# Kernel tuning notes

Hardware: AMD Instinct MI355X
Metric: run time of the kernel (lower is better)

The kernel has to match this reference:

```python
import jax, jax.numpy as jnp
import numpy as np

B, S, I, F = 2048, 512, 256, 256  # batch, seq_length, input_size, filter_num


def setup_inputs() -> dict:
    key = jax.random.key(0)
    ks = jax.random.split(key, 9)
    sc = 0.05
    return {
        "hidden": jax.random.normal(ks[0], (B, I), jnp.float32),
        "inp": jax.random.normal(ks[1], (B, S, I), jnp.float32),
        "W1": jax.random.normal(ks[2], (F, I), jnp.float32) * sc,   # linear1 weight (no bias)
        "Wc": jax.random.normal(ks[3], (F, S), jnp.float32) * sc,   # conv kernel [F,1,S,1] squeezed
        "bc": jax.random.normal(ks[4], (F,), jnp.float32) * sc,     # conv bias
        "W2": jax.random.normal(ks[5], (I, I + F), jnp.float32) * sc,
        "b2": jax.random.normal(ks[6], (I,), jnp.float32) * sc,
        "Wfc": jax.random.normal(ks[7], (1, I), jnp.float32) * sc,
        "bfc": jax.random.normal(ks[8], (1,), jnp.float32) * sc,
    }


def reference(hidden, inp, W1, Wc, bc, W2, b2, Wfc, bfc):
    # w = linear1(hidden).unsqueeze(1): [B,1,F]
    w = hidden @ W1.T  # [B,F]
    # Conv2d(1,F,kernel=(S,1)) over input [B,1,S,I] -> [B,F,1,I]; kernel spans full
    # time axis with width 1, so it's a contraction over t per input channel i.
    Hc_raw = jnp.einsum('bti,ft->bfi', inp, Wc) + bc[None, :, None]  # [B,F,I]
    # faithful to torch: .squeeze().reshape([-1, input_size, filter_num])
    H_c = Hc_raw.reshape(-1, I, F)  # [B,I,F]
    s = jnp.sum(H_c * w[:, None, :], axis=2)          # [B,I]
    a = jax.nn.sigmoid(s)
    v = jnp.sum(a[:, :, None] * H_c, axis=1)          # [B,F]
    concat = jnp.concatenate([hidden, v], axis=1)     # [B,I+F]
    h_prime = concat @ W2.T + b2                      # [B,I]
    out = h_prime @ Wfc.T + bfc                       # [B,1]
    return out
```

## Files before the change

kernel.cpp:

```cpp
#include <hip/hip_runtime.h>

#define B_ 2048
#define S_ 512
#define I_ 256
#define F_ 256
#define NG 8

#define OFF_W    0
#define OFF_SW   (OFF_W + B_*F_)
#define OFF_U    (OFF_SW + B_)
#define OFF_P    (OFF_U + B_*S_)
#define OFF_RP   (OFF_P + B_*S_)

__global__ __launch_bounds__(256) void k_pre(
    const float* __restrict__ hidden, const float* __restrict__ W1,
    const float* __restrict__ W2, const float* __restrict__ Wfc,
    float* __restrict__ ws) {
  const int tid = threadIdx.x;

  if (blockIdx.x >= B_ / 4) {
    const int g = blockIdx.x - B_ / 4;
    float acc0 = 0.f, acc1 = 0.f;
#pragma unroll 8
    for (int ii = 0; ii < 32; ++ii) {
      const int i = g * 32 + ii;
      const float f = Wfc[i];
      acc0 += f * W2[(size_t)i * (I_ + F_) + tid];
      acc1 += f * W2[(size_t)i * (I_ + F_) + tid + 256];
    }
    ws[OFF_RP + g * 512 + tid] = acc0;
    ws[OFF_RP + g * 512 + 256 + tid] = acc1;
    return;
  }

  __shared__ float h[4][I_];
  __shared__ float red[256];
  const int b0 = blockIdx.x * 4;
#pragma unroll
  for (int k = 0; k < 4; ++k) h[k][tid] = hidden[(size_t)(b0 + k) * I_ + tid];
  __syncthreads();

  const int f = tid;
  const float4* wrow = (const float4*)(W1 + (size_t)f * I_);
  float acc[4] = {0.f, 0.f, 0.f, 0.f};
#pragma unroll 4
  for (int iq = 0; iq < I_ / 4; ++iq) {
    const float4 v = wrow[iq];
    const int i = 4 * iq;
#pragma unroll
    for (int k = 0; k < 4; ++k)
      acc[k] += v.x * h[k][i] + v.y * h[k][i + 1] + v.z * h[k][i + 2] + v.w * h[k][i + 3];
  }
#pragma unroll
  for (int k = 0; k < 4; ++k) ws[OFF_W + (size_t)(b0 + k) * F_ + f] = acc[k];

#pragma unroll
  for (int k = 0; k < 4; ++k) {
    red[tid] = acc[k];
    __syncthreads();
    for (int s = 128; s > 0; s >>= 1) { if (tid < s) red[tid] += red[tid + s]; __syncthreads(); }
    if (tid == 0) ws[OFF_SW + b0 + k] = red[0];
    __syncthreads();
  }
}

__global__ __launch_bounds__(256) void k1_scan(
    const float* __restrict__ inp, const float* __restrict__ wsw,
    const float* __restrict__ wsrp,
    float* __restrict__ wsu, float* __restrict__ wsp) {
  const int ROWS = 32;
  const int b = blockIdx.y;
  const int t0 = blockIdx.x * ROWS;
  const int tid = threadIdx.x;
  const int lane = tid & 63;
  const int wid = tid >> 6;

  __shared__ float rv_lds[F_];
  float rv = 0.f;
#pragma unroll
  for (int g = 0; g < NG; ++g) rv += wsrp[g * 512 + 256 + tid];
  rv_lds[tid] = rv;
  __syncthreads();

  const float4 w4  = ((const float4*)(wsw + (size_t)b * F_))[lane];
  const float4 rv4 = ((const float4*)rv_lds)[lane];
  const float* base = inp + ((size_t)b * S_ + t0) * I_;
  float* uo = wsu + (size_t)b * S_ + t0;
  float* po = wsp + (size_t)b * S_ + t0;

#pragma unroll
  for (int rr = 0; rr < ROWS / 4; ++rr) {
    const int row = wid + 4 * rr;
    const float4 in4 = ((const float4*)(base + (size_t)row * I_))[lane];
    float du = in4.x * w4.x + in4.y * w4.y + in4.z * w4.z + in4.w * w4.w;
    float dp = in4.x * rv4.x + in4.y * rv4.y + in4.z * rv4.z + in4.w * rv4.w;
#pragma unroll
    for (int m = 32; m >= 1; m >>= 1) {
      du += __shfl_xor(du, m, 64);
      dp += __shfl_xor(dp, m, 64);
    }
    if (lane == 0) { uo[row] = du; po[row] = dp; }
  }
}

__global__ __launch_bounds__(256) void k2_epilogue(
    const float* __restrict__ Wc, const float* __restrict__ bc,
    const float* __restrict__ b2, const float* __restrict__ Wfc,
    const float* __restrict__ bfc, const float* __restrict__ hidden,
    const float* __restrict__ wsu, const float* __restrict__ wsp,
    const float* __restrict__ wsSw, const float* __restrict__ wsrp,
    float* __restrict__ out) {
  const int b0 = blockIdx.x * 4;
  const int tid = threadIdx.x;
  const int lane = tid & 63;
  const int wid = tid >> 6;
  __shared__ float u[4][S_];
  __shared__ float p[4][S_];
  __shared__ float redA[4], redB[4];
  __shared__ float wred[4][4];

  float rh = 0.f, rv = 0.f;
#pragma unroll
  for (int g = 0; g < NG; ++g) {
    rh += wsrp[g * 512 + tid];
    rv += wsrp[g * 512 + 256 + tid];
  }
  float t0 = rv, t1 = Wfc[tid] * b2[tid];
#pragma unroll
  for (int m = 32; m >= 1; m >>= 1) {
    t0 += __shfl_xor(t0, m, 64);
    t1 += __shfl_xor(t1, m, 64);
  }
  if (lane == 0) { redA[wid] = t0; redB[wid] = t1; }

#pragma unroll
  for (int k = 0; k < 4; ++k) {
    u[k][tid]       = wsu[(size_t)(b0 + k) * S_ + tid];
    u[k][tid + 256] = wsu[(size_t)(b0 + k) * S_ + tid + 256];
    p[k][tid]       = wsp[(size_t)(b0 + k) * S_ + tid];
    p[k][tid + 256] = wsp[(size_t)(b0 + k) * S_ + tid + 256];
  }
  __syncthreads();

  const float R  = redA[0] + redA[1] + redA[2] + redA[3];
  const float c0 = redB[0] + redB[1] + redB[2] + redB[3] + bfc[0];

  const int x = tid;
  const float4* wrow = (const float4*)(Wc + (size_t)x * S_);
  float ss[4] = {0.f, 0.f, 0.f, 0.f};
  float qs[4] = {0.f, 0.f, 0.f, 0.f};
#pragma unroll 4
  for (int tq = 0; tq < S_ / 4; ++tq) {
    const float4 v = wrow[tq];
    const int t = 4 * tq;
#pragma unroll
    for (int k = 0; k < 4; ++k) {
      ss[k] += v.x * u[k][t] + v.y * u[k][t + 1] + v.z * u[k][t + 2] + v.w * u[k][t + 3];
      qs[k] += v.x * p[k][t] + v.y * p[k][t + 1] + v.z * p[k][t + 2] + v.w * p[k][t + 3];
    }
  }

  const float bcx = bc[x];
#pragma unroll
  for (int k = 0; k < 4; ++k) {
    const float Sw = wsSw[b0 + k];
    const float s = ss[k] + bcx * Sw;
    const float a = 1.f / (1.f + expf(-s));
    float partial = a * (qs[k] + bcx * R) + rh * hidden[(size_t)(b0 + k) * I_ + x];
#pragma unroll
    for (int m = 32; m >= 1; m >>= 1) partial += __shfl_xor(partial, m, 64);
    if (lane == 0) wred[k][wid] = partial;
  }
  __syncthreads();
  if (tid < 4)
    out[b0 + tid] = wred[tid][0] + wred[tid][1] + wred[tid][2] + wred[tid][3] + c0;
}

extern "C" void kernel_launch(void* const* d_in, const int* in_sizes, int n_in,
                              void* d_out, int out_size, void* d_ws, size_t ws_size,
                              hipStream_t stream) {
  (void)in_sizes; (void)n_in; (void)out_size; (void)ws_size;
  const float* hidden = (const float*)d_in[0];
  const float* inp    = (const float*)d_in[1];
  const float* W1     = (const float*)d_in[2];
  const float* Wc     = (const float*)d_in[3];
  const float* bc     = (const float*)d_in[4];
  const float* W2     = (const float*)d_in[5];
  const float* b2     = (const float*)d_in[6];
  const float* Wfc    = (const float*)d_in[7];
  const float* bfc    = (const float*)d_in[8];
  float* out = (float*)d_out;
  float* ws  = (float*)d_ws;

  hipLaunchKernelGGL(k_pre, dim3(B_ / 4 + NG), dim3(256), 0, stream,
                     hidden, W1, W2, Wfc, ws);
  hipLaunchKernelGGL(k1_scan, dim3(S_ / 32, B_), dim3(256), 0, stream,
                     inp, ws + OFF_W, ws + OFF_RP, ws + OFF_U, ws + OFF_P);
  hipLaunchKernelGGL(k2_epilogue, dim3(B_ / 4), dim3(256), 0, stream,
                     Wc, bc, b2, Wfc, bfc, hidden,
                     ws + OFF_U, ws + OFF_P, ws + OFF_SW, ws + OFF_RP, out);
}
```

Before: 263.1 us.

## Retile epilogue to 8 batches per block with 8x8 register tiles

After: 284.9 us. 8.3% more time.

```diff
diff --git a/kernel.cpp b/kernel.cpp
--- a/kernel.cpp
+++ b/kernel.cpp
@@ -110,14 +110,18 @@
     const float* __restrict__ wsu, const float* __restrict__ wsp,
     const float* __restrict__ wsSw, const float* __restrict__ wsrp,
     float* __restrict__ out) {
-  const int b0 = blockIdx.x * 4;
+  const int b0 = blockIdx.x * 8;
   const int tid = threadIdx.x;
+  const int tk  = tid & 7;
+  const int txg = tid >> 3;
   const int lane = tid & 63;
   const int wid = tid >> 6;
-  __shared__ float u[4][S_];
-  __shared__ float p[4][S_];
+
+  __shared__ float u_lds[8][516];
+  __shared__ float p_lds[8][516];
+  __shared__ float rh_lds[256];
   __shared__ float redA[4], redB[4];
-  __shared__ float wred[4][4];
+  __shared__ float wred[4][8];
 
   float rh = 0.f, rv = 0.f;
 #pragma unroll
@@ -125,55 +129,64 @@
     rh += wsrp[g * 512 + tid];
     rv += wsrp[g * 512 + 256 + tid];
   }
-  float t0 = rv, t1 = Wfc[tid] * b2[tid];
+  rh_lds[tid] = rh;
+
+  float t0r = rv, t1r = Wfc[tid] * b2[tid];
 #pragma unroll
   for (int m = 32; m >= 1; m >>= 1) {
-    t0 += __shfl_xor(t0, m, 64);
-    t1 += __shfl_xor(t1, m, 64);
-  }
-  if (lane == 0) { redA[wid] = t0; redB[wid] = t1; }
-
-#pragma unroll
-  for (int k = 0; k < 4; ++k) {
-    u[k][tid]       = wsu[(size_t)(b0 + k) * S_ + tid];
-    u[k][tid + 256] = wsu[(size_t)(b0 + k) * S_ + tid + 256];
-    p[k][tid]       = wsp[(size_t)(b0 + k) * S_ + tid];
-    p[k][tid + 256] = wsp[(size_t)(b0 + k) * S_ + tid + 256];
+    t0r += __shfl_xor(t0r, m, 64);
+    t1r += __shfl_xor(t1r, m, 64);
+  }
+  if (lane == 0) { redA[wid] = t0r; redB[wid] = t1r; }
+
+  for (int idx = tid; idx < 8 * S_; idx += 256) {
+    const int k = idx >> 9, t = idx & (S_ - 1);
+    u_lds[k][t] = wsu[(size_t)(b0 + k) * S_ + t];
+    p_lds[k][t] = wsp[(size_t)(b0 + k) * S_ + t];
   }
   __syncthreads();
 
   const float R  = redA[0] + redA[1] + redA[2] + redA[3];
   const float c0 = redB[0] + redB[1] + redB[2] + redB[3] + bfc[0];
 
-  const int x = tid;
-  const float4* wrow = (const float4*)(Wc + (size_t)x * S_);
-  float ss[4] = {0.f, 0.f, 0.f, 0.f};
-  float qs[4] = {0.f, 0.f, 0.f, 0.f};
-#pragma unroll 4
-  for (int tq = 0; tq < S_ / 4; ++tq) {
-    const float4 v = wrow[tq];
-    const int t = 4 * tq;
-#pragma unroll
-    for (int k = 0; k < 4; ++k) {
-      ss[k] += v.x * u[k][t] + v.y * u[k][t + 1] + v.z * u[k][t + 2] + v.w * u[k][t + 3];
-      qs[k] += v.x * p[k][t] + v.y * p[k][t + 1] + v.z * p[k][t + 2] + v.w * p[k][t + 3];
+  float ss[8] = {0.f,0.f,0.f,0.f,0.f,0.f,0.f,0.f};
+  float qs[8] = {0.f,0.f,0.f,0.f,0.f,0.f,0.f,0.f};
+  const float* wcbase = Wc + (size_t)txg * 8 * S_;
+
+#pragma unroll 2
+  for (int t = 0; t < S_; t += 4) {
+    const float4 u4 = *(const float4*)&u_lds[tk][t];
+    const float4 p4 = *(const float4*)&p_lds[tk][t];
+#pragma unroll
+    for (int j = 0; j < 8; ++j) {
+      const float4 w4 = *(const float4*)(wcbase + (size_t)j * S_ + t);
+      ss[j] += w4.x * u4.x + w4.y * u4.y + w4.z * u4.z + w4.w * u4.w;
+      qs[j] += w4.x * p4.x + w4.y * p4.y + w4.z * p4.z + w4.w * p4.w;
     }
   }
 
-  const float bcx = bc[x];
-#pragma unroll
-  for (int k = 0; k < 4; ++k) {
-    const float Sw = wsSw[b0 + k];
-    const float s = ss[k] + bcx * Sw;
+  const float Sw = wsSw[b0 + tk];
+  const float4 bca = *(const float4*)(bc + txg * 8);
+  const float4 bcb = *(const float4*)(bc + txg * 8 + 4);
+  const float4 hda = *(const float4*)(hidden + (size_t)(b0 + tk) * I_ + txg * 8);
+  const float4 hdb = *(const float4*)(hidden + (size_t)(b0 + tk) * I_ + txg * 8 + 4);
+  const float bcv[8] = {bca.x, bca.y, bca.z, bca.w, bcb.x, bcb.y, bcb.z, bcb.w};
+  const float hdv[8] = {hda.x, hda.y, hda.z, hda.w, hdb.x, hdb.y, hdb.z, hdb.w};
+
+  float tot = 0.f;
+#pragma unroll
+  for (int j = 0; j < 8; ++j) {
+    const float s = ss[j] + bcv[j] * Sw;
     const float a = 1.f / (1.f + expf(-s));
-    float partial = a * (qs[k] + bcx * R) + rh * hidden[(size_t)(b0 + k) * I_ + x];
-#pragma unroll
-    for (int m = 32; m >= 1; m >>= 1) partial += __shfl_xor(partial, m, 64);
-    if (lane == 0) wred[k][wid] = partial;
-  }
-  __syncthreads();
-  if (tid < 4)
-    out[b0 + tid] = wred[tid][0] + wred[tid][1] + wred[tid][2] + wred[tid][3] + c0;
+    tot += a * (qs[j] + bcv[j] * R) + rh_lds[txg * 8 + j] * hdv[j];
+  }
+  tot += __shfl_xor(tot, 8, 64);
+  tot += __shfl_xor(tot, 16, 64);
+  tot += __shfl_xor(tot, 32, 64);
+  if (lane < 8) wred[wid][lane] = tot;
+  __syncthreads();
+  if (tid < 8)
+    out[b0 + tid] = wred[0][tid] + wred[1][tid] + wred[2][tid] + wred[3][tid] + c0;
 }
 
 extern "C" void kernel_launch(void* const* d_in, const int* in_sizes, int n_in,
@@ -196,7 +209,7 @@
                      hidden, W1, W2, Wfc, ws);
   hipLaunchKernelGGL(k1_scan, dim3(S_ / 32, B_), dim3(256), 0, stream,
                      inp, ws + OFF_W, ws + OFF_RP, ws + OFF_U, ws + OFF_P);
-  hipLaunchKernelGGL(k2_epilogue, dim3(B_ / 4), dim3(256), 0, stream,
+  hipLaunchKernelGGL(k2_epilogue, dim3(B_ / 8), dim3(256), 0, stream,
                      Wc, bc, b2, Wfc, bfc, hidden,
                      ws + OFF_U, ws + OFF_P, ws + OFF_SW, ws + OFF_RP, out);
 }
```
